# Optimization experiments

Hardware: AMD Instinct MI355X
Metric: run time of the kernel (lower is better)

## Reference

```python
import jax, jax.numpy as jnp
import numpy as np

KNN = 8


def setup_inputs() -> dict:
    key = jax.random.key(0)
    ks = jax.random.split(key, 13)
    B, C, H, W, k = 8, 256, 128, 128, 16
    g = max(8, C // 4)  # c_reduced = 64
    stdv = 1.0 / np.sqrt(g)
    return {
        "x": jax.random.normal(ks[0], (B, C, H, W), jnp.float32),
        "U": jax.random.normal(ks[1], (B, H, k), jnp.float32),
        "S": jax.random.uniform(ks[2], (B, k), jnp.float32),
        "V": jax.random.normal(ks[3], (B, C, k), jnp.float32),
        "G": jax.random.normal(ks[4], (H * W, H), jnp.float32) / np.sqrt(H),
        "w_row": jax.random.normal(ks[5], (H,), jnp.float32),
        "w_col": jax.random.normal(ks[6], (W,), jnp.float32),
        "boast": jax.random.normal(ks[7], (H + W + C,), jnp.float32),
        "res_scale": jnp.float32(1.0),
        "reduce_w": jax.random.normal(ks[8], (g, C // g), jnp.float32) * 0.1,
        "gcn_w": jax.random.uniform(ks[9], (g, g), jnp.float32, -stdv, stdv),
        "gcn_b": jax.random.uniform(ks[10], (g,), jnp.float32, -stdv, stdv),
        "expand_w": jax.random.normal(ks[11], (g, C // g), jnp.float32) * 0.1,
    }


def _gcn_extract(x, U, reduce_w, gcn_w, gcn_b, expand_w):
    # GCNExtractor: mean over W -> grouped 1x1 reduce -> KNN-GCN -> grouped expand -> broadcast over W
    B, C, H, W = x.shape
    g, m = reduce_w.shape  # groups, in-channels-per-group (C = g*m)
    X_node = x.mean(axis=3)                                 # (B, C, H)
    X_red = jnp.einsum('bgmh,gm->bhg', X_node.reshape(B, g, m, H), reduce_w)  # (B, H, g)
    # build_knn_adj (batched): cosine sim + topk + symmetric degree normalization
    Un = U / jnp.clip(jnp.linalg.norm(U, axis=-1, keepdims=True), 1e-12)
    sim = jnp.einsum('bik,bjk->bij', Un, Un)                # (B, H, H)
    k_use = min(KNN, H)
    vals, idx = jax.lax.top_k(sim, k_use)                   # (B, H, k_use)
    deg = vals.sum(-1)                                      # row-sum of sparse A
    dinv = deg ** -0.5
    dinv_col = jnp.take_along_axis(jnp.broadcast_to(dinv[:, None, :], sim.shape), idx, axis=-1)
    vals_n = vals * dinv[:, :, None] * dinv_col
    b_idx = jnp.arange(B)[:, None, None]
    r_idx = jnp.arange(H)[None, :, None]
    adj = jnp.zeros((B, H, H), x.dtype).at[b_idx, r_idx, idx].set(vals_n)
    # GCNConv (the torch code densifies adj anyway)
    support = jnp.einsum('bhg,gd->bhd', X_red, gcn_w)
    out = jax.nn.relu(jnp.einsum('bij,bjd->bid', adj, support) + gcn_b)   # (B, H, g)
    out = jnp.einsum('bhg,gm->bgmh', out, expand_w).reshape(B, C, H)      # grouped expand
    return jnp.broadcast_to(out[..., None], (B, C, H, W))


def _globalatt(x, U, S, V, G, w_row, w_col, boast, res_scale,
               reduce_w, gcn_w, gcn_b, expand_w):
    B, C, H, W = x.shape
    topo = _gcn_extract(x, U, reduce_w, gcn_w, gcn_b, expand_w)
    topo_map = jnp.abs(topo).sum(axis=1)
    topo_map = topo_map / jnp.clip(topo_map.reshape(B, -1).max(axis=1), 1e-6)[:, None, None]
    Usum = U.sum(-1)                                       # (B, H); einsum('bhk,bw->bhwk').sum(-1)
    logits_row = Usum[:, :, None] * w_row[None, None, :] + 0.5 * topo_map
    att_row = jax.nn.softmax(logits_row, axis=-1)
    R = jnp.einsum('bhw,bchw->bch', att_row, x)
    row_out = jnp.einsum('bch,ph->bcp', R, G).reshape(B, C, H, W)   # Gt = G.T
    logits_col = Usum[:, :, None] * w_col[None, None, :] + 0.5 * topo_map
    att_col = jax.nn.softmax(logits_col, axis=1)
    Cctx = jnp.einsum('bhw,bchw->bcw', att_col, x)
    col_out = jnp.einsum('bcw,pw->bcp', Cctx, G).reshape(B, C, H, W)
    # channel branch
    z_x = x.mean(axis=(2, 3))
    z_topo = topo.mean(axis=(2, 3))
    z_k = jnp.einsum('bc,bck->bk', z_x, V) + 0.5 * jnp.einsum('bc,bck->bk', z_topo, V)
    zS = z_k[:, :, None] * S[:, None, :]                   # (B, k, k)
    ch_rec1 = jnp.einsum('bck,kj->?', V, zS) if False else jnp.einsum('bck,bkj->bcj', V, zS)
    ch_rec2 = jnp.einsum('bck,bjk->bcj', V, zS)
    ch_rec = jnp.concatenate([ch_rec1, ch_rec2], axis=-1).mean(axis=-1)
    chan_out = x * jax.nn.sigmoid(ch_rec)[:, :, None, None]
    # topo branch
    topo_channel = topo.mean(axis=(2, 3), keepdims=True)
    topo_branch = jax.nn.softmax(topo_channel, axis=1) * topo \
        + jax.nn.sigmoid(topo.mean(axis=1, keepdims=True)) * topo
    # fusion weights
    s_input = jnp.concatenate([S, jnp.broadcast_to(w_col[None], (B, W)),
                               jnp.broadcast_to(w_row[None], (B, H))], axis=1)
    w4 = jax.nn.softmax(jnp.einsum('bp,c->bc', s_input, boast), axis=-1)
    a_row, a_col, a_chan = w4[:, :H], w4[:, H:H + W], w4[:, H + W:]
    a_topo = a_row[:, :, None] * a_col[:, None, :]          # (B, H, W)
    out = (a_row[:, None, :, None] * row_out
           + a_col[:, None, None, :] * col_out
           + a_chan[:, :, None, None] * chan_out
           + a_topo[:, None, :, :] * topo_branch)
    return res_scale * x + out


def reference(x, U, S, V, G, w_row, w_col, boast, res_scale,
              reduce_w, gcn_w, gcn_b, expand_w):
    return _globalatt(x, U, S, V, G, w_row, w_col, boast, res_scale,
                      reduce_w, gcn_w, gcn_b, expand_w)
```

## Files before the change

kernel.cpp:

```cpp
#include <hip/hip_runtime.h>
#include <math.h>

#define BB 8
#define CC 256
#define HH 128
#define WW 128
#define PP 16384

typedef __attribute__((ext_vector_type(8))) short bf16x8;
typedef __attribute__((ext_vector_type(4))) float f32x4;

#define O_XNODE   0u
#define O_T       262144u
#define O_R       524288u
#define O_CTX     786432u
#define O_GT      1048576u
#define O_ATTR    3145728u
#define O_ATTC    3276800u
#define O_UN      3407872u
#define O_SUP     3424256u
#define O_VALS    3555328u
#define O_DEG     3563520u
#define O_USUM    3564544u
#define O_TMSUM   3565568u
#define O_TM      3566592u
#define O_SIGMT   3567616u
#define O_ALPHA   3568640u
#define O_SC      3570688u
#define O_AROW    3572736u
#define O_ACOL    3573760u
#define O_IDX     3574784u

__device__ __forceinline__ ushort f2b(float f) {
    unsigned u = __float_as_uint(f);
    unsigned r = (u + 0x7FFFu + ((u >> 16) & 1u)) >> 16;
    return (ushort)r;
}

__device__ __forceinline__ float bredSum256(float v, float* red) {
    int t = threadIdx.x, lane = t & 63, wv = t >> 6;
    for (int o = 32; o; o >>= 1) v += __shfl_xor(v, o);
    __syncthreads();
    if (lane == 0) red[wv] = v;
    __syncthreads();
    return red[0] + red[1] + red[2] + red[3];
}
__device__ __forceinline__ float bredMax256(float v, float* red) {
    int t = threadIdx.x, lane = t & 63, wv = t >> 6;
    for (int o = 32; o; o >>= 1) v = fmaxf(v, __shfl_xor(v, o));
    __syncthreads();
    if (lane == 0) red[wv] = v;
    __syncthreads();
    return fmaxf(fmaxf(red[0], red[1]), fmaxf(red[2], red[3]));
}

__global__ __launch_bounds__(256) void kA(const float* __restrict__ x, float* __restrict__ Xnode,
                                          const float* __restrict__ G, ushort* __restrict__ Gb) {
    if (blockIdx.x < 1024) {
        int i = (blockIdx.x * 256 + threadIdx.x) * 8;
        float4 v0 = *(const float4*)&G[i];
        float4 v1 = *(const float4*)&G[i + 4];
        union { ushort us[8]; uint4 u4; } o;
        o.us[0] = f2b(v0.x); o.us[1] = f2b(v0.y); o.us[2] = f2b(v0.z); o.us[3] = f2b(v0.w);
        o.us[4] = f2b(v1.x); o.us[5] = f2b(v1.y); o.us[6] = f2b(v1.z); o.us[7] = f2b(v1.w);
        *(uint4*)&Gb[i] = o.u4;
        return;
    }
    int bid = blockIdx.x - 1024;
    int t = threadIdx.x;
    int row = bid * 32 + (t >> 3);
    int seg = t & 7;
    const float4* p = (const float4*)&x[(size_t)row * 128 + seg * 16];
    float4 a = p[0], b4 = p[1], c4 = p[2], d4 = p[3];
    float s = ((a.x + a.y) + (a.z + a.w)) + ((b4.x + b4.y) + (b4.z + b4.w))
            + ((c4.x + c4.y) + (c4.z + c4.w)) + ((d4.x + d4.y) + (d4.z + d4.w));
    s += __shfl_xor(s, 1, 8);
    s += __shfl_xor(s, 2, 8);
    s += __shfl_xor(s, 4, 8);
    if (seg == 0) Xnode[row] = s * (1.0f / 128.0f);
}

__global__ __launch_bounds__(64) void kS1(const float* __restrict__ U, const float* __restrict__ Xnode,
                                          const float* __restrict__ reduce_w, const float* __restrict__ gcn_w,
                                          float* __restrict__ Un, float* __restrict__ Usum, float* __restrict__ sup) {
    int bh = blockIdx.x; int b = bh >> 7, h = bh & 127;
    int t = threadIdx.x;
    __shared__ float xr[64];
    float u = (t < 16) ? U[bh * 16 + t] : 0.f;
    float ss = u * u;
    for (int o = 8; o; o >>= 1) ss += __shfl_xor(ss, o, 16);
    float us = u;
    for (int o = 8; o; o >>= 1) us += __shfl_xor(us, o, 16);
    if (t < 16) Un[bh * 16 + t] = u / fmaxf(sqrtf(ss), 1e-12f);
    if (t == 0) Usum[bh] = us;
    float acc = 0.f;
    #pragma unroll
    for (int m = 0; m < 4; ++m)
        acc = fmaf(Xnode[((b * CC + t * 4 + m) << 7) + h], reduce_w[t * 4 + m], acc);
    xr[t] = acc;
    __syncthreads();
    float sp = 0.f;
    for (int g = 0; g < 64; ++g) sp = fmaf(xr[g], gcn_w[g * 64 + t], sp);
    sup[bh * 64 + t] = sp;
}

__global__ __launch_bounds__(128) void kS2(const float* __restrict__ Un, float* __restrict__ vals,
                                           int* __restrict__ idxv, float* __restrict__ deg) {
    int bh = blockIdx.x; int b = bh >> 7;
    int t = threadIdx.x;
    __shared__ float uni[16];
    __shared__ unsigned long long wmax[2];
    if (t < 16) uni[t] = Un[bh * 16 + t];
    __syncthreads();
    const float* uj = Un + (b << 11) + t * 16;
    float s = 0.f;
    #pragma unroll
    for (int q = 0; q < 16; ++q) s = fmaf(uni[q], uj[q], s);
    float dsum = 0.f;
    for (int r = 0; r < 8; ++r) {
        unsigned m = __float_as_uint(s);
        m = (m & 0x80000000u) ? ~m : (m | 0x80000000u);
        unsigned long long key = ((unsigned long long)m << 32) | (unsigned)(0xFFFFFFFFu - (unsigned)t);
        for (int o = 32; o; o >>= 1) { unsigned long long ok = __shfl_xor(key, o); key = key > ok ? key : ok; }
        if ((t & 63) == 0) wmax[t >> 6] = key;
        __syncthreads();
        unsigned long long kk = wmax[0] > wmax[1] ? wmax[0] : wmax[1];
        __syncthreads();
        int jw = (int)(0xFFFFFFFFu - (unsigned)(kk & 0xFFFFFFFFu));
        unsigned mm = (unsigned)(kk >> 32);
        mm = (mm & 0x80000000u) ? (mm & 0x7FFFFFFFu) : ~mm;
        float vw = __uint_as_float(mm);
        dsum += vw;
        if (t == r) { vals[bh * 8 + r] = vw; idxv[bh * 8 + r] = jw; }
        if (t == jw) s = -3.4e38f;
    }
    if (t == 0) deg[bh] = dsum;
}

__global__ __launch_bounds__(64) void kS3(const float* __restrict__ vals, const int* __restrict__ idxv,
                                          const float* __restrict__ deg, const float* __restrict__ sup,
                                          const float* __restrict__ gcn_b, const float* __restrict__ expand_w,
                                          float* __restrict__ Tg,
                                          float* __restrict__ tmsum, float* __restrict__ sigmt) {
    int bh = blockIdx.x; int b = bh >> 7, i = bh & 127;
    int t = threadIdx.x;
    __shared__ float coef[8];
    __shared__ int id[8];
    if (t < 8) {
        int j = idxv[bh * 8 + t];
        float dv = vals[bh * 8 + t] * (1.f / sqrtf(deg[bh])) * (1.f / sqrtf(deg[(b << 7) + j]));
        coef[t] = dv; id[t] = j;
    }
    __syncthreads();
    float acc = gcn_b[t];
    #pragma unroll
    for (int q = 0; q < 8; ++q) acc = fmaf(coef[q], sup[((b << 7) + id[q]) * 64 + t], acc);
    float go = fmaxf(acc, 0.f);
    float e0 = expand_w[t * 4], e1 = expand_w[t * 4 + 1], e2 = expand_w[t * 4 + 2], e3 = expand_w[t * 4 + 3];
    Tg[((b * CC + t * 4 + 0) << 7) + i] = go * e0;
    Tg[((b * CC + t * 4 + 1) << 7) + i] = go * e1;
    Tg[((b * CC + t * 4 + 2) << 7) + i] = go * e2;
    Tg[((b * CC + t * 4 + 3) << 7) + i] = go * e3;
    float tms = fabsf(go) * (fabsf(e0) + fabsf(e1) + fabsf(e2) + fabsf(e3));
    float mtp = go * (e0 + e1 + e2 + e3);
    for (int o = 32; o; o >>= 1) { tms += __shfl_down(tms, o); mtp += __shfl_down(mtp, o); }
    if (t == 0) {
        tmsum[bh] = tms;
        sigmt[bh] = 1.f / (1.f + expf(-(mtp * (1.f / 256.f))));
    }
}

__global__ __launch_bounds__(256) void kS4(const float* __restrict__ Xnode, const float* __restrict__ Tg,
                                           const float* __restrict__ V, const float* __restrict__ S,
                                           const float* __restrict__ boast, const float* __restrict__ res_scale,
                                           const float* __restrict__ w_row, const float* __restrict__ w_col,
                                           const float* __restrict__ tmsum,
                                           float* __restrict__ tm, float* __restrict__ alpha, float* __restrict__ sc,
                                           float* __restrict__ arow, float* __restrict__ acol) {
    int b = blockIdx.x; int t = threadIdx.x;
    __shared__ float red[4];
    __shared__ float zc[256];
    __shared__ float zk[16];
    float tv = (t < 128) ? tmsum[(b << 7) + t] : -3.4e38f;
    float tmax = bredMax256(tv, red);
    if (t < 128) tm[(b << 7) + t] = tv / fmaxf(tmax, 1e-6f);
    const float* xn = Xnode + ((size_t)(b * CC + t) << 7);
    const float* tg = Tg + ((size_t)(b * CC + t) << 7);
    float zx = 0.f, zt = 0.f;
    for (int h = 0; h < 128; h += 4) {
        float4 a = *(const float4*)&xn[h];
        float4 bq = *(const float4*)&tg[h];
        zx += (a.x + a.y) + (a.z + a.w);
        zt += (bq.x + bq.y) + (bq.z + bq.w);
    }
    zx *= (1.f / 128.f); zt *= (1.f / 128.f);
    zc[t] = zx + 0.5f * zt;
    __syncthreads();
    if (t < 16) {
        float a = 0.f;
        for (int c = 0; c < 256; ++c) a = fmaf(zc[c], V[((b * CC + c) << 4) + t], a);
        zk[t] = a;
    }
    __syncthreads();
    float sumS = 0.f, sumz = 0.f;
    #pragma unroll
    for (int j = 0; j < 16; ++j) { sumS += S[(b << 4) + j]; sumz += zk[j]; }
    float Vz = 0.f, VS = 0.f;
    #pragma unroll
    for (int j = 0; j < 16; ++j) {
        float vv = V[((b * CC + t) << 4) + j];
        Vz = fmaf(vv, zk[j], Vz);
        VS = fmaf(vv, S[(b << 4) + j], VS);
    }
    float ch = (Vz * sumS + VS * sumz) * (1.f / 32.f);
    float sig = 1.f / (1.f + expf(-ch));
    float zm = bredMax256(zt, red);
    float e = expf(zt - zm);
    float es = bredSum256(e, red);
    sc[b * CC + t] = e / es;
    float ps = 0.f;
    for (int q = t; q < 272; q += 256) {
        float si = (q < 16) ? S[(b << 4) + q] : (q < 144 ? w_col[q - 16] : w_row[q - 144]);
        ps += si;
    }
    float ssum = bredSum256(ps, red);
    float l0 = ssum * boast[t];
    float l1 = ssum * boast[256 + t];
    float lm = bredMax256(fmaxf(l0, l1), red);
    float e0 = expf(l0 - lm), e1 = expf(l1 - lm);
    float esum = bredSum256(e0 + e1, red);
    float w40 = e0 / esum, w41 = e1 / esum;
    if (t < 128) arow[(b << 7) + t] = w40;
    else acol[(b << 7) + (t - 128)] = w40;
    alpha[b * CC + t] = res_scale[0] + w41 * sig;
}

__global__ __launch_bounds__(128) void kS5(const float* __restrict__ Usum, const float* __restrict__ w_row,
                                           const float* __restrict__ w_col, const float* __restrict__ tm,
                                           float* __restrict__ attr, float* __restrict__ attc) {
    __shared__ float red[2];
    int id = blockIdx.x;
    int t = threadIdx.x;
    if (id < BB * HH) {
        int bh = id;
        float l = Usum[bh] * w_row[t] + 0.5f * tm[bh];
        float m = l;
        for (int o = 32; o; o >>= 1) m = fmaxf(m, __shfl_xor(m, o));
        if ((t & 63) == 0) red[t >> 6] = m;
        __syncthreads();
        m = fmaxf(red[0], red[1]);
        __syncthreads();
        float e = expf(l - m);
        float s = e;
        for (int o = 32; o; o >>= 1) s += __shfl_xor(s, o);
        if ((t & 63) == 0) red[t >> 6] = s;
        __syncthreads();
        s = red[0] + red[1];
        attr[id * 128 + t] = e / s;
    } else {
        int bw = id - BB * HH; int b = bw >> 7, w = bw & 127;
        float l = Usum[(b << 7) + t] * w_col[w] + 0.5f * tm[(b << 7) + t];
        float m = l;
        for (int o = 32; o; o >>= 1) m = fmaxf(m, __shfl_xor(m, o));
        if ((t & 63) == 0) red[t >> 6] = m;
        __syncthreads();
        m = fmaxf(red[0], red[1]);
        __syncthreads();
        float e = expf(l - m);
        float s = e;
        for (int o = 32; o; o >>= 1) s += __shfl_xor(s, o);
        if ((t & 63) == 0) red[t >> 6] = s;
        __syncthreads();
        s = red[0] + red[1];
        attc[((b << 7) + t) * 128 + w] = e / s;
    }
}

__global__ __launch_bounds__(256) void kR(const float* __restrict__ x, const float* __restrict__ attr,
                                          const float* __restrict__ attc, ushort* __restrict__ Rh,
                                          ushort* __restrict__ Ch) {
    int bc = blockIdx.x;
    int b = bc >> 8;
    int t = threadIdx.x;
    __shared__ float tile[64][132];
    __shared__ float rsum[64][5];
    __shared__ float cred[8][128];
    int wq = (t & 31) * 4;
    int hg = t >> 5;
    const float* xb  = x    + (size_t)bc * PP;
    const float* arb = attr + (size_t)b * PP;
    const float* acb = attc + (size_t)b * PP;
    float4 cacc = make_float4(0.f, 0.f, 0.f, 0.f);
    #pragma unroll
    for (int cchunk = 0; cchunk < 2; ++cchunk) {
        int h0 = cchunk * 64;
        #pragma unroll
        for (int i = 0; i < 8; ++i) {
            int hh = i * 8 + hg;
            int off = (h0 + hh) * 128 + wq;
            float4 xv  = *(const float4*)&xb[off];
            float4 ar4 = *(const float4*)&arb[off];
            float4 ac4 = *(const float4*)&acb[off];
            cacc.x = fmaf(ac4.x, xv.x, cacc.x);
            cacc.y = fmaf(ac4.y, xv.y, cacc.y);
            cacc.z = fmaf(ac4.z, xv.z, cacc.z);
            cacc.w = fmaf(ac4.w, xv.w, cacc.w);
            float4 pr;
            pr.x = ar4.x * xv.x; pr.y = ar4.y * xv.y; pr.z = ar4.z * xv.z; pr.w = ar4.w * xv.w;
            *(float4*)&tile[hh][wq] = pr;
        }
        __syncthreads();
        int hl = t & 63, q = t >> 6;
        float s = 0.f;
        #pragma unroll
        for (int j = 0; j < 8; ++j) {
            float4 v = *(const float4*)&tile[hl][q * 32 + j * 4];
            s += (v.x + v.y) + (v.z + v.w);
        }
        rsum[hl][q] = s;
        __syncthreads();
        if (t < 64) Rh[bc * 128 + h0 + t] = f2b(rsum[t][0] + rsum[t][1] + rsum[t][2] + rsum[t][3]);
        __syncthreads();
    }
    *(float4*)&cred[hg][wq] = cacc;
    __syncthreads();
    if (t < 128) {
        float s = 0.f;
        #pragma unroll
        for (int g = 0; g < 8; ++g) s += cred[g][t];
        Ch[bc * 128 + t] = f2b(s);
    }
}

__global__ __launch_bounds__(256) void kF(const float* __restrict__ x, const ushort* __restrict__ Rh,
                                          const ushort* __restrict__ Ch, const ushort* __restrict__ Gb,
                                          const float* __restrict__ Tg, const float* __restrict__ alpha,
                                          const float* __restrict__ sc, const float* __restrict__ sigmt,
                                          const float* __restrict__ arow, const float* __restrict__ acol,
                                          float* __restrict__ out) {
    __shared__ ushort gL[16384];
    __shared__ ushort rL[8192];
    __shared__ ushort cL[8192];
    int b = blockIdx.z;
    int c0 = blockIdx.y * 64;
    int p0 = blockIdx.x * 128;
    int tid = threadIdx.x;
    int wid = tid >> 6, l = tid & 63;
    int lr = l & 15, lk = l >> 4;
    int pbase = p0 + (wid & 1) * 64;
    int cwave = (wid >> 1) * 32;
    int h = blockIdx.x;

    f32x4 xv[2][4];
    float al[2], scv[2], tgv[2];
    size_t rowb[2];
    #pragma unroll
    for (int n = 0; n < 2; ++n) {
        int c = c0 + cwave + 16 * n + lr;
        rowb[n] = ((size_t)((b << 8) + c) << 14) + pbase + 4 * lk;
        #pragma unroll
        for (int m = 0; m < 4; ++m)
            xv[n][m] = *(const f32x4*)&x[rowb[n] + 16 * m];
        al[n] = alpha[(b << 8) + c];
        scv[n] = sc[(b << 8) + c];
        tgv[n] = Tg[(((b << 8) + c) << 7) + h];
    }
    float ar = arow[(b << 7) + h];
    float smt = sigmt[(b << 7) + h];
    int wloc = (wid & 1) * 64 + 4 * lk;
    f32x4 acw[4];
    #pragma unroll
    for (int m = 0; m < 4; ++m) acw[m] = *(const f32x4*)&acol[(b << 7) + wloc + 16 * m];

    {
        const uint4* gsrc = (const uint4*)(Gb + (size_t)p0 * 128);
        #pragma unroll
        for (int it = 0; it < 8; ++it) {
            int j = it * 256 + tid;
            uint4 v = gsrc[j];
            int row = j >> 4, col16 = j & 15;
            *(uint4*)&gL[row * 128 + ((col16 ^ (row & 7)) << 3)] = v;
        }
        const uint4* rsrc = (const uint4*)(Rh + (((b << 8) + c0) << 7));
        const uint4* csrc = (const uint4*)(Ch + (((b << 8) + c0) << 7));
        #pragma unroll
        for (int it = 0; it < 4; ++it) {
            int j = it * 256 + tid;
            uint4 vr = rsrc[j];
            uint4 vc = csrc[j];
            int row = j >> 4, col16 = j & 15;
            int d = row * 128 + ((col16 ^ (row & 7)) << 3);
            *(uint4*)&rL[d] = vr;
            *(uint4*)&cL[d] = vc;
        }
    }
    __syncthreads();

    f32x4 accR[4][2], accC[4][2];
    #pragma unroll
    for (int m = 0; m < 4; ++m)
        #pragma unroll
        for (int n = 0; n < 2; ++n) {
            accR[m][n] = (f32x4){0.f, 0.f, 0.f, 0.f};
            accC[m][n] = (f32x4){0.f, 0.f, 0.f, 0.f};
        }

    int swz = lr & 7;
    int growb = (wid & 1) * 64 + lr;
    int crowb = cwave + lr;
    #pragma unroll
    for (int ks = 0; ks < 4; ++ks) {
        int col = ((ks * 4 + lk) ^ swz) << 3;
        bf16x8 ag0 = *(const bf16x8*)&gL[(growb +  0) * 128 + col];
        bf16x8 ag1 = *(const bf16x8*)&gL[(growb + 16) * 128 + col];
        bf16x8 ag2 = *(const bf16x8*)&gL[(growb + 32) * 128 + col];
        bf16x8 ag3 = *(const bf16x8*)&gL[(growb + 48) * 128 + col];
        bf16x8 bR0 = *(const bf16x8*)&rL[(crowb +  0) * 128 + col];
        bf16x8 bR1 = *(const bf16x8*)&rL[(crowb + 16) * 128 + col];
        bf16x8 bC0 = *(const bf16x8*)&cL[(crowb +  0) * 128 + col];
        bf16x8 bC1 = *(const bf16x8*)&cL[(crowb + 16) * 128 + col];
        accR[0][0] = __builtin_amdgcn_mfma_f32_16x16x32_bf16(ag0, bR0, accR[0][0], 0, 0, 0);
        accR[0][1] = __builtin_amdgcn_mfma_f32_16x16x32_bf16(ag0, bR1, accR[0][1], 0, 0, 0);
        accR[1][0] = __builtin_amdgcn_mfma_f32_16x16x32_bf16(ag1, bR0, accR[1][0], 0, 0, 0);
        accR[1][1] = __builtin_amdgcn_mfma_f32_16x16x32_bf16(ag1, bR1, accR[1][1], 0, 0, 0);
        accR[2][0] = __builtin_amdgcn_mfma_f32_16x16x32_bf16(ag2, bR0, accR[2][0], 0, 0, 0);
        accR[2][1] = __builtin_amdgcn_mfma_f32_16x16x32_bf16(ag2, bR1, accR[2][1], 0, 0, 0);
        accR[3][0] = __builtin_amdgcn_mfma_f32_16x16x32_bf16(ag3, bR0, accR[3][0], 0, 0, 0);
        accR[3][1] = __builtin_amdgcn_mfma_f32_16x16x32_bf16(ag3, bR1, accR[3][1], 0, 0, 0);
        accC[0][0] = __builtin_amdgcn_mfma_f32_16x16x32_bf16(ag0, bC0, accC[0][0], 0, 0, 0);
        accC[0][1] = __builtin_amdgcn_mfma_f32_16x16x32_bf16(ag0, bC1, accC[0][1], 0, 0, 0);
        accC[1][0] = __builtin_amdgcn_mfma_f32_16x16x32_bf16(ag1, bC0, accC[1][0], 0, 0, 0);
        accC[1][1] = __builtin_amdgcn_mfma_f32_16x16x32_bf16(ag1, bC1, accC[1][1], 0, 0, 0);
        accC[2][0] = __builtin_amdgcn_mfma_f32_16x16x32_bf16(ag2, bC0, accC[2][0], 0, 0, 0);
        accC[2][1] = __builtin_amdgcn_mfma_f32_16x16x32_bf16(ag2, bC1, accC[2][1], 0, 0, 0);
        accC[3][0] = __builtin_amdgcn_mfma_f32_16x16x32_bf16(ag3, bC0, accC[3][0], 0, 0, 0);
        accC[3][1] = __builtin_amdgcn_mfma_f32_16x16x32_bf16(ag3, bC1, accC[3][1], 0, 0, 0);
    }

    #pragma unroll
    for (int n = 0; n < 2; ++n) {
        float tb = (scv[n] + smt) * tgv[n];
        #pragma unroll
        for (int m = 0; m < 4; ++m) {
            f32x4 o;
            o[0] = fmaf(al[n], xv[n][m][0], fmaf(ar, accR[m][n][0], fmaf(acw[m][0], accC[m][n][0], ar * acw[m][0] * tb)));
            o[1] = fmaf(al[n], xv[n][m][1], fmaf(ar, accR[m][n][1], fmaf(acw[m][1], accC[m][n][1], ar * acw[m][1] * tb)));
            o[2] = fmaf(al[n], xv[n][m][2], fmaf(ar, accR[m][n][2], fmaf(acw[m][2], accC[m][n][2], ar * acw[m][2] * tb)));
            o[3] = fmaf(al[n], xv[n][m][3], fmaf(ar, accR[m][n][3], fmaf(acw[m][3], accC[m][n][3], ar * acw[m][3] * tb)));
            *(f32x4*)&out[rowb[n] + 16 * m] = o;
        }
    }
}

extern "C" void kernel_launch(void* const* d_in, const int* in_sizes, int n_in,
                              void* d_out, int out_size, void* d_ws, size_t ws_size,
                              hipStream_t stream) {
    const float* x        = (const float*)d_in[0];
    const float* U        = (const float*)d_in[1];
    const float* S        = (const float*)d_in[2];
    const float* V        = (const float*)d_in[3];
    const float* G        = (const float*)d_in[4];
    const float* w_row    = (const float*)d_in[5];
    const float* w_col    = (const float*)d_in[6];
    const float* boast    = (const float*)d_in[7];
    const float* res_scale= (const float*)d_in[8];
    const float* reduce_w = (const float*)d_in[9];
    const float* gcn_w    = (const float*)d_in[10];
    const float* gcn_b    = (const float*)d_in[11];
    const float* expand_w = (const float*)d_in[12];
    float* ws = (float*)d_ws;
    float* out = (float*)d_out;

    float* Xnode = ws + O_XNODE;
    float* Tg    = ws + O_T;
    ushort* Rh   = (ushort*)(ws + O_R);
    ushort* Ch   = (ushort*)(ws + O_CTX);
    ushort* Gb   = (ushort*)(ws + O_GT);
    float* attr  = ws + O_ATTR;
    float* attc  = ws + O_ATTC;
    float* Un    = ws + O_UN;
    float* sup   = ws + O_SUP;
    float* vals  = ws + O_VALS;
    float* deg   = ws + O_DEG;
    float* Usum  = ws + O_USUM;
    float* tmsum = ws + O_TMSUM;
    float* tm    = ws + O_TM;
    float* sigmt = ws + O_SIGMT;
    float* alpha = ws + O_ALPHA;
    float* sc    = ws + O_SC;
    float* arow  = ws + O_AROW;
    float* acol  = ws + O_ACOL;
    int*   idxv  = (int*)(ws + O_IDX);

    kA<<<1024 + BB * CC * HH / 32, 256, 0, stream>>>(x, Xnode, G, Gb);
    kS1<<<BB * HH, 64, 0, stream>>>(U, Xnode, reduce_w, gcn_w, Un, Usum, sup);
    kS2<<<BB * HH, 128, 0, stream>>>(Un, vals, idxv, deg);
    kS3<<<BB * HH, 64, 0, stream>>>(vals, idxv, deg, sup, gcn_b, expand_w, Tg, tmsum, sigmt);
    kS4<<<BB, 256, 0, stream>>>(Xnode, Tg, V, S, boast, res_scale, w_row, w_col, tmsum,
                                tm, alpha, sc, arow, acol);
    kS5<<<BB * HH + BB * WW, 128, 0, stream>>>(Usum, w_row, w_col, tm, attr, attc);
    kR<<<BB * CC, 256, 0, stream>>>(x, attr, attc, Rh, Ch);
    kF<<<dim3(PP / 128, CC / 64, BB), 256, 0, stream>>>(x, Rh, Ch, Gb, Tg, alpha, sc, sigmt,
                                                        arow, acol, out);
}
```

Measured before the change: 148.0 us.

## Fuse KNN normalization into top-k kernel and precompute column softmax stats

```diff
diff --git a/kernel.cpp b/kernel.cpp
--- a/kernel.cpp
+++ b/kernel.cpp
@@ -9,6 +9,7 @@
 
 typedef __attribute__((ext_vector_type(8))) short bf16x8;
 typedef __attribute__((ext_vector_type(4))) float f32x4;
+typedef unsigned long long ull;
 
 #define O_XNODE   0u
 #define O_T       262144u
@@ -17,7 +18,8 @@
 #define O_GT      1048576u
 #define O_ATTR    3145728u
 #define O_ATTC    3276800u
-#define O_UN      3407872u
+#define O_MCOL    3407872u
+#define O_SCOL    3408896u
 #define O_SUP     3424256u
 #define O_VALS    3555328u
 #define O_DEG     3563520u
@@ -80,39 +82,41 @@
     if (seg == 0) Xnode[row] = s * (1.0f / 128.0f);
 }
 
-__global__ __launch_bounds__(64) void kS1(const float* __restrict__ U, const float* __restrict__ Xnode,
-                                          const float* __restrict__ reduce_w, const float* __restrict__ gcn_w,
-                                          float* __restrict__ Un, float* __restrict__ Usum, float* __restrict__ sup) {
-    int bh = blockIdx.x; int b = bh >> 7, h = bh & 127;
+__global__ __launch_bounds__(128) void kS12(const float* __restrict__ U, const float* __restrict__ Xnode,
+                                            const float* __restrict__ reduce_w, const float* __restrict__ gcn_w,
+                                            float* __restrict__ Usum, float* __restrict__ sup,
+                                            float* __restrict__ vals, int* __restrict__ idxv,
+                                            float* __restrict__ deg) {
+    int bh = blockIdx.x; int b = bh >> 7, i = bh & 127;
     int t = threadIdx.x;
+    __shared__ float UnL[128][17];
     __shared__ float xr[64];
-    float u = (t < 16) ? U[bh * 16 + t] : 0.f;
-    float ss = u * u;
-    for (int o = 8; o; o >>= 1) ss += __shfl_xor(ss, o, 16);
-    float us = u;
-    for (int o = 8; o; o >>= 1) us += __shfl_xor(us, o, 16);
-    if (t < 16) Un[bh * 16 + t] = u / fmaxf(sqrtf(ss), 1e-12f);
-    if (t == 0) Usum[bh] = us;
-    float acc = 0.f;
-    #pragma unroll
-    for (int m = 0; m < 4; ++m)
-        acc = fmaf(Xnode[((b * CC + t * 4 + m) << 7) + h], reduce_w[t * 4 + m], acc);
-    xr[t] = acc;
-    __syncthreads();
-    float sp = 0.f;
-    for (int g = 0; g < 64; ++g) sp = fmaf(xr[g], gcn_w[g * 64 + t], sp);
-    sup[bh * 64 + t] = sp;
-}
-
-__global__ __launch_bounds__(128) void kS2(const float* __restrict__ Un, float* __restrict__ vals,
-                                           int* __restrict__ idxv, float* __restrict__ deg) {
-    int bh = blockIdx.x; int b = bh >> 7;
-    int t = threadIdx.x;
-    __shared__ float uni[16];
-    __shared__ unsigned long long wmax[2];
-    if (t < 16) uni[t] = Un[bh * 16 + t];
-    __syncthreads();
-    const float* uj = Un + (b << 11) + t * 16;
+    __shared__ ull wmax[2];
+
+    float u[16]; float ss = 0.f, us = 0.f;
+    const float* up = U + (((b << 7) + t) << 4);
+    #pragma unroll
+    for (int q = 0; q < 16; ++q) { u[q] = up[q]; ss = fmaf(u[q], u[q], ss); us += u[q]; }
+    float inv = 1.f / fmaxf(sqrtf(ss), 1e-12f);
+    #pragma unroll
+    for (int q = 0; q < 16; ++q) UnL[t][q] = u[q] * inv;
+    if (i == 0) Usum[(b << 7) + t] = us;
+    if (t < 64) {
+        float acc = 0.f;
+        #pragma unroll
+        for (int m = 0; m < 4; ++m)
+            acc = fmaf(Xnode[((b * CC + t * 4 + m) << 7) + i], reduce_w[t * 4 + m], acc);
+        xr[t] = acc;
+    }
+    __syncthreads();
+    if (t < 64) {
+        float sp = 0.f;
+        for (int g = 0; g < 64; ++g) sp = fmaf(xr[g], gcn_w[g * 64 + t], sp);
+        sup[bh * 64 + t] = sp;
+    }
+    float uni[16], uj[16];
+    #pragma unroll
+    for (int q = 0; q < 16; ++q) { uni[q] = UnL[i][q]; uj[q] = UnL[t][q]; }
     float s = 0.f;
     #pragma unroll
     for (int q = 0; q < 16; ++q) s = fmaf(uni[q], uj[q], s);
@@ -120,13 +124,13 @@
     for (int r = 0; r < 8; ++r) {
         unsigned m = __float_as_uint(s);
         m = (m & 0x80000000u) ? ~m : (m | 0x80000000u);
-        unsigned long long key = ((unsigned long long)m << 32) | (unsigned)(0xFFFFFFFFu - (unsigned)t);
-        for (int o = 32; o; o >>= 1) { unsigned long long ok = __shfl_xor(key, o); key = key > ok ? key : ok; }
+        ull key = ((ull)m << 32) | (unsigned)(0xFFFFFFFFu - (unsigned)t);
+        for (int o = 32; o; o >>= 1) { ull ok = __shfl_xor(key, o); key = key > ok ? key : ok; }
         if ((t & 63) == 0) wmax[t >> 6] = key;
         __syncthreads();
-        unsigned long long kk = wmax[0] > wmax[1] ? wmax[0] : wmax[1];
+        ull kk = wmax[0] > wmax[1] ? wmax[0] : wmax[1];
         __syncthreads();
-        int jw = (int)(0xFFFFFFFFu - (unsigned)(kk & 0xFFFFFFFFu));
+        int jw = (int)(0xFFFFFFFFu - (unsigned)(kk & 0xFFFFFFFFull));
         unsigned mm = (unsigned)(kk >> 32);
         mm = (mm & 0x80000000u) ? (mm & 0x7FFFFFFFu) : ~mm;
         float vw = __uint_as_float(mm);
@@ -174,16 +178,24 @@
                                            const float* __restrict__ V, const float* __restrict__ S,
                                            const float* __restrict__ boast, const float* __restrict__ res_scale,
                                            const float* __restrict__ w_row, const float* __restrict__ w_col,
-                                           const float* __restrict__ tmsum,
+                                           const float* __restrict__ tmsum, const float* __restrict__ Usum,
                                            float* __restrict__ tm, float* __restrict__ alpha, float* __restrict__ sc,
-                                           float* __restrict__ arow, float* __restrict__ acol) {
+                                           float* __restrict__ arow, float* __restrict__ acol,
+                                           float* __restrict__ mcol, float* __restrict__ scol) {
     int b = blockIdx.x; int t = threadIdx.x;
     __shared__ float red[4];
     __shared__ float zc[256];
     __shared__ float zk[16];
+    __shared__ float UsL[128], wcL[128], tmlocL[128];
     float tv = (t < 128) ? tmsum[(b << 7) + t] : -3.4e38f;
     float tmax = bredMax256(tv, red);
-    if (t < 128) tm[(b << 7) + t] = tv / fmaxf(tmax, 1e-6f);
+    if (t < 128) {
+        float tmv = tv / fmaxf(tmax, 1e-6f);
+        tm[(b << 7) + t] = tmv;
+        tmlocL[t] = tmv;
+        UsL[t] = Usum[(b << 7) + t];
+        wcL[t] = w_col[t];
+    }
     const float* xn = Xnode + ((size_t)(b * CC + t) << 7);
     const float* tg = Tg + ((size_t)(b * CC + t) << 7);
     float zx = 0.f, zt = 0.f;
@@ -233,47 +245,45 @@
     if (t < 128) arow[(b << 7) + t] = w40;
     else acol[(b << 7) + (t - 128)] = w40;
     alpha[b * CC + t] = res_scale[0] + w41 * sig;
+    __syncthreads();
+    if (t < 128) {
+        float wc = wcL[t];
+        float m = -3.4e38f;
+        #pragma unroll 4
+        for (int h = 0; h < 128; ++h) m = fmaxf(m, fmaf(UsL[h], wc, 0.5f * tmlocL[h]));
+        float sacc = 0.f;
+        #pragma unroll 4
+        for (int h = 0; h < 128; ++h) sacc += expf(fmaf(UsL[h], wc, 0.5f * tmlocL[h]) - m);
+        mcol[(b << 7) + t] = m;
+        scol[(b << 7) + t] = sacc;
+    }
 }
 
 __global__ __launch_bounds__(128) void kS5(const float* __restrict__ Usum, const float* __restrict__ w_row,
                                            const float* __restrict__ w_col, const float* __restrict__ tm,
+                                           const float* __restrict__ mcol, const float* __restrict__ scol,
                                            float* __restrict__ attr, float* __restrict__ attc) {
     __shared__ float red[2];
-    int id = blockIdx.x;
+    int bh = blockIdx.x; int b = bh >> 7;
     int t = threadIdx.x;
-    if (id < BB * HH) {
-        int bh = id;
-        float l = Usum[bh] * w_row[t] + 0.5f * tm[bh];
-        float m = l;
-        for (int o = 32; o; o >>= 1) m = fmaxf(m, __shfl_xor(m, o));
-        if ((t & 63) == 0) red[t >> 6] = m;
-        __syncthreads();
-        m = fmaxf(red[0], red[1]);
-        __syncthreads();
-        float e = expf(l - m);
-        float s = e;
-        for (int o = 32; o; o >>= 1) s += __shfl_xor(s, o);
-        if ((t & 63) == 0) red[t >> 6] = s;
-        __syncthreads();
-        s = red[0] + red[1];
-        attr[id * 128 + t] = e / s;
-    } else {
-        int bw = id - BB * HH; int b = bw >> 7, w = bw & 127;
-        float l = Usum[(b << 7) + t] * w_col[w] + 0.5f * tm[(b << 7) + t];
-        float m = l;
-        for (int o = 32; o; o >>= 1) m = fmaxf(m, __shfl_xor(m, o));
-        if ((t & 63) == 0) red[t >> 6] = m;
-        __syncthreads();
-        m = fmaxf(red[0], red[1]);
-        __syncthreads();
-        float e = expf(l - m);
-        float s = e;
-        for (int o = 32; o; o >>= 1) s += __shfl_xor(s, o);
-        if ((t & 63) == 0) red[t >> 6] = s;
-        __syncthreads();
-        s = red[0] + red[1];
-        attc[((b << 7) + t) * 128 + w] = e / s;
-    }
+    float us = Usum[bh];
+    float tmh = 0.5f * tm[bh];
+    float l = fmaf(us, w_row[t], tmh);
+    float m = l;
+    for (int o = 32; o; o >>= 1) m = fmaxf(m, __shfl_xor(m, o));
+    if ((t & 63) == 0) red[t >> 6] = m;
+    __syncthreads();
+    m = fmaxf(red[0], red[1]);
+    __syncthreads();
+    float e = expf(l - m);
+    float s = e;
+    for (int o = 32; o; o >>= 1) s += __shfl_xor(s, o);
+    if ((t & 63) == 0) red[t >> 6] = s;
+    __syncthreads();
+    s = red[0] + red[1];
+    attr[bh * 128 + t] = e / s;
+    float lc = fmaf(us, w_col[t], tmh);
+    attc[bh * 128 + t] = expf(lc - mcol[(b << 7) + t]) / scol[(b << 7) + t];
 }
 
 __global__ __launch_bounds__(256) void kR(const float* __restrict__ x, const float* __restrict__ attr,
@@ -478,7 +488,8 @@
     ushort* Gb   = (ushort*)(ws + O_GT);
     float* attr  = ws + O_ATTR;
     float* attc  = ws + O_ATTC;
-    float* Un    = ws + O_UN;
+    float* mcol  = ws + O_MCOL;
+    float* scol  = ws + O_SCOL;
     float* sup   = ws + O_SUP;
     float* vals  = ws + O_VALS;
     float* deg   = ws + O_DEG;
@@ -493,12 +504,11 @@
     int*   idxv  = (int*)(ws + O_IDX);
 
     kA<<<1024 + BB * CC * HH / 32, 256, 0, stream>>>(x, Xnode, G, Gb);
-    kS1<<<BB * HH, 64, 0, stream>>>(U, Xnode, reduce_w, gcn_w, Un, Usum, sup);
-    kS2<<<BB * HH, 128, 0, stream>>>(Un, vals, idxv, deg);
+    kS12<<<BB * HH, 128, 0, stream>>>(U, Xnode, reduce_w, gcn_w, Usum, sup, vals, idxv, deg);
     kS3<<<BB * HH, 64, 0, stream>>>(vals, idxv, deg, sup, gcn_b, expand_w, Tg, tmsum, sigmt);
-    kS4<<<BB, 256, 0, stream>>>(Xnode, Tg, V, S, boast, res_scale, w_row, w_col, tmsum,
-                                tm, alpha, sc, arow, acol);
-    kS5<<<BB * HH + BB * WW, 128, 0, stream>>>(Usum, w_row, w_col, tm, attr, attc);
+    kS4<<<BB, 256, 0, stream>>>(Xnode, Tg, V, S, boast, res_scale, w_row, w_col, tmsum, Usum,
+                                tm, alpha, sc, arow, acol, mcol, scol);
+    kS5<<<BB * HH, 128, 0, stream>>>(Usum, w_row, w_col, tm, mcol, scol, attr, attc);
     kR<<<BB * CC, 256, 0, stream>>>(x, attr, attc, Rh, Ch);
     kF<<<dim3(PP / 128, CC / 64, BB), 256, 0, stream>>>(x, Rh, Ch, Gb, Tg, alpha, sc, sigmt,
                                                         arow, acol, out);
```

Result: slower. 156.3 us (+5.6%).
